# Kernel optimization log

Measured on AMD Instinct MI355X. Metric: run time of the kernel, lower is better.

## Reference

```python
import jax, jax.numpy as jnp
import numpy as np

N = 256          # num agents
HID = 128        # hidden_dim
ACT = 5          # action_dim
NH = 4           # num_heads
D = HID + 16     # concat_hidden_dim = 144
E = D * NH       # mha embed dim = 576
HD = D           # per-head dim = E // NH = 144
OBS_RX, OBS_RY = 4, 2   # obs_r from fov_size=(9,5)
GRID = 40


def setup_inputs() -> dict:
    key = jax.random.key(0)
    ks = jax.random.split(key, 24)
    g = lambda k, shape, s: (jax.random.normal(k, shape, dtype=jnp.float32) * s)
    inp = {
        "hidden_state_n": g(ks[0], (N, HID), 1.0),
        "action_n": g(ks[1], (N, HID), 1.0),
        "state_n": jax.random.randint(ks[2], (N, 2), 0, GRID, dtype=jnp.int32),
        # obs encoder
        "W_enc": g(ks[3], (HID, 16), HID ** -0.5), "b_enc": jnp.zeros((16,), jnp.float32),
        # MHABlock outer projections
        "Wq": g(ks[4], (D, E), D ** -0.5), "bq": jnp.zeros((E,), jnp.float32),
        "Wk": g(ks[5], (D, E), D ** -0.5), "bk": jnp.zeros((E,), jnp.float32),
        "Wv": g(ks[6], (D, E), D ** -0.5), "bv": jnp.zeros((E,), jnp.float32),
        # nn.MultiheadAttention internal in/out projections
        "Wiq": g(ks[7], (E, E), E ** -0.5), "biq": jnp.zeros((E,), jnp.float32),
        "Wik": g(ks[8], (E, E), E ** -0.5), "bik": jnp.zeros((E,), jnp.float32),
        "Wiv": g(ks[9], (E, E), E ** -0.5), "biv": jnp.zeros((E,), jnp.float32),
        "Wo_proj": g(ks[10], (E, E), E ** -0.5), "bo_proj": jnp.zeros((E,), jnp.float32),
        "W_O": g(ks[11], (E, D), E ** -0.5),  # no bias
        # dueling decoders
        "W_val": g(ks[12], (D, 1), D ** -0.5), "b_val": jnp.zeros((1,), jnp.float32),
        "W_adv": g(ks[13], (D, ACT), D ** -0.5), "b_adv": jnp.zeros((ACT,), jnp.float32),
    }
    return inp


def reference(hidden_state_n, action_n, W_enc, b_enc, Wq, bq, Wk, bk, Wv, bv,
              Wiq, biq, Wik, bik, Wiv, biv, Wo_proj, bo_proj, W_O,
              W_val, b_val, W_adv, b_adv, state_n):
    n = hidden_state_n.shape[0]
    # observed_agents[i] = {j > i : |x_i-x_j|<=rx and |y_i-y_j|<=ry}
    pos = state_n.astype(jnp.int32)
    dx = jnp.abs(pos[:, None, 0] - pos[None, :, 0])
    dy = jnp.abs(pos[:, None, 1] - pos[None, :, 1])
    upper = jnp.arange(n)[None, :] > jnp.arange(n)[:, None]
    mask = (dx <= OBS_RX) & (dy <= OBS_RY) & upper            # [N,N], mask[i,j]: j observed by i

    # per-neighbor feature c_j = concat(obs_encoder(h_j), a_j)  -> [N, D]
    obs = hidden_state_n @ W_enc + b_enc                       # [N,16]
    C = jnp.concatenate([obs, action_n], axis=-1)              # [N,D]

    # MHABlock: outer Q/K/V projections then nn.MultiheadAttention
    q = (C @ Wq + bq) @ Wiq + biq                              # [N,E]
    k = (C @ Wk + bk) @ Wik + bik
    v = (C @ Wv + bv) @ Wiv + biv
    q2 = q.reshape(n, NH, HD)
    k2 = k.reshape(n, NH, HD)
    v2 = v.reshape(n, NH, HD)

    scale = 1.0 / np.sqrt(HD).astype(np.float32)
    S = jnp.einsum("jhd,khd->hjk", q2, k2) * scale             # [H,N,N] shared across agents

    pair = (mask[:, None, :, None] & mask[:, None, None, :])   # [N,1,Nq,Nk]
    logits = jnp.where(pair, S[None, :, :, :], -1e9)           # [N,H,N,N]
    m = jnp.max(logits, axis=-1, keepdims=True)
    p = jnp.exp(logits - m) * pair.astype(logits.dtype)
    attn = p / jnp.maximum(p.sum(axis=-1, keepdims=True), 1e-9)

    ctx = jnp.einsum("ihjk,khd->ijhd", attn, v2).reshape(n, n, E)  # [N,Nq,E]
    out = (ctx @ Wo_proj + bo_proj) @ W_O                          # [N,Nq,D]

    # sum over the (masked) neighbor/query axis -> per-agent h_i
    h = jnp.sum(out * mask[:, :, None].astype(out.dtype), axis=1)  # [N,D]

    V = h @ W_val + b_val                                          # [N,1]
    A = h @ W_adv + b_adv                                          # [N,ACT]
    Q = V + A - jnp.mean(A, axis=-1, keepdims=True)                # dueling Q
    return Q
```

## Files before the change

kernel.cpp:

```cpp
#include <hip/hip_runtime.h>
#include <hip/hip_bf16.h>

#define NAG 256
#define HID 128
#define ACT 5
#define NH 4
#define DD 144
#define EE 576
#define HDIM 144
#define CMAX 20

template<int KDIM, int AG, int NX, int GSLOTS>
__global__ __launch_bounds__(256) void k_gemmK(
    const float* __restrict__ A0, const float* __restrict__ A1, const float* __restrict__ A2,
    const float* __restrict__ W0, const float* __restrict__ W1, const float* __restrict__ W2,
    const float* __restrict__ bb0, const float* __restrict__ bb1, const float* __restrict__ bb2,
    const float* __restrict__ bscale,
    float* __restrict__ o0, float* __restrict__ o1, float* __restrict__ o2,
    int N)
{
    constexpr int Kc = KDIM / 4;
    constexpr int G  = 36;
    constexpr int NG = Kc / G;
    constexpr int LDA = KDIM + 4;
    __shared__ union { float As[8 * LDA]; float red[2048]; } sm;

    const int p = blockIdx.x;
    const int xcd = p & 7, qq = p >> 3;
    const int mb = qq & 31, gslot = qq >> 5;
    const int g = xcd + 8 * gslot;
    if (g >= AG) return;
    const int bx = g % NX, z = g / NX;
    const float* A   = (z == 0) ? A0  : (z == 1) ? A1  : A2;
    const float* W   = (z == 0) ? W0  : (z == 1) ? W1  : W2;
    const float* bia = (z == 0) ? bb0 : (z == 1) ? bb1 : bb2;
    float*       out = (z == 0) ? o0  : (z == 1) ? o1  : o2;
    const int tid = threadIdx.x;

    for (int idx = tid; idx < 8 * (KDIM / 4); idx += 256) {
        int r = idx / (KDIM / 4), c = idx % (KDIM / 4);
        *((float4*)&sm.As[r * LDA + c * 4]) =
            *(const float4*)(A + (size_t)(mb * 8 + r) * KDIM + c * 4);
    }
    __syncthreads();

    const int wave = tid >> 6, lane = tid & 63;
    const int colg = bx * 64 + lane;
    const bool cv = colg < N;
    const int colc = cv ? colg : (N - 1);
    const float* Wp = W + (size_t)(wave * Kc) * N + colc;
    float acc[8] = {};
    float wv[G], wn[G];
    #pragma unroll
    for (int j = 0; j < G; ++j) wv[j] = Wp[(size_t)j * N];
    for (int gi = 0; gi < NG; ++gi) {
        if (gi + 1 < NG) {
            const float* Wn = Wp + (size_t)(gi + 1) * G * N;
            #pragma unroll
            for (int j = 0; j < G; ++j) wn[j] = Wn[(size_t)j * N];
        }
        const int kb = wave * Kc + gi * G;
        #pragma unroll
        for (int j4 = 0; j4 < G / 4; ++j4) {
            #pragma unroll
            for (int r = 0; r < 8; ++r) {
                float4 a4 = *(const float4*)&sm.As[r * LDA + kb + j4 * 4];
                acc[r] += a4.x * wv[j4 * 4 + 0] + a4.y * wv[j4 * 4 + 1]
                        + a4.z * wv[j4 * 4 + 2] + a4.w * wv[j4 * 4 + 3];
            }
        }
        #pragma unroll
        for (int j = 0; j < G; ++j) wv[j] = wn[j];
    }
    __syncthreads();
    #pragma unroll
    for (int r = 0; r < 8; ++r) sm.red[wave * 512 + r * 64 + lane] = acc[r];
    __syncthreads();
    #pragma unroll
    for (int q = 0; q < 2; ++q) {
        int idx = tid + q * 256;
        int r = idx >> 6, cl = idx & 63;
        int col = bx * 64 + cl;
        if (col < N) {
            float s = sm.red[idx] + sm.red[512 + idx]
                    + sm.red[1024 + idx] + sm.red[1536 + idx];
            int row = mb * 8 + r;
            float bs = bscale ? bscale[row] : 1.f;
            float bb = bia ? bia[col] : 0.f;
            out[(size_t)row * N + col] = s + bs * bb;
        }
    }
}

__global__ __launch_bounds__(256) void k_gemm1(
    const float* __restrict__ hidden, const float* __restrict__ action,
    const float* __restrict__ W_enc, const float* __restrict__ b_enc,
    const float* __restrict__ Wq, const float* __restrict__ Wk, const float* __restrict__ Wv,
    const float* __restrict__ bq, const float* __restrict__ bk, const float* __restrict__ bv,
    float* __restrict__ tq, float* __restrict__ tk, float* __restrict__ tv)
{
    const int p = blockIdx.x;
    const int xcd = p & 7, qq = p >> 3;
    const int mb = qq & 31, gslot = qq >> 5;
    const int g = xcd + 8 * gslot;
    if (g >= 27) return;
    const int bx = g % 9, z = g / 9;
    const float* W  = (z == 0) ? Wq : (z == 1) ? Wk : Wv;
    const float* bi = (z == 0) ? bq : (z == 1) ? bk : bv;
    float*      out = (z == 0) ? tq : (z == 1) ? tk : tv;
    const int tid = threadIdx.x;

    __shared__ float Ct[8][148];
    __shared__ union { struct { float Hs[8][132]; float We[2048]; } e;
                       float red[2048]; } u;
    {
        int r = tid >> 5, kq = tid & 31;
        *((float4*)&u.e.Hs[r][kq * 4]) =
            *(const float4*)(hidden + (mb * 8 + r) * HID + kq * 4);
        *((float4*)&Ct[r][16 + kq * 4]) =
            *(const float4*)(action + (mb * 8 + r) * HID + kq * 4);
        *((float4*)&u.e.We[tid * 4])        = *(const float4*)(W_enc + tid * 4);
        *((float4*)&u.e.We[1024 + tid * 4]) = *(const float4*)(W_enc + 1024 + tid * 4);
    }
    __syncthreads();
    if (tid < 128) {
        int r = tid >> 4, o = tid & 15;
        float acc = 0.f;
        #pragma unroll 8
        for (int d = 0; d < HID; ++d) acc += u.e.Hs[r][d] * u.e.We[d * 16 + o];
        Ct[r][o] = acc + b_enc[o];
    }
    __syncthreads();

    constexpr int Kc = 36, G = 36;
    const int wave = tid >> 6, lane = tid & 63;
    const int colg = bx * 64 + lane;
    const float* Wp = W + (size_t)(wave * Kc) * EE + colg;
    float acc[8] = {};
    float wv[G];
    #pragma unroll
    for (int j = 0; j < G; ++j) wv[j] = Wp[(size_t)j * EE];
    const int kb = wave * Kc;
    #pragma unroll
    for (int j4 = 0; j4 < G / 4; ++j4) {
        #pragma unroll
        for (int r = 0; r < 8; ++r) {
            float4 a4 = *(const float4*)&Ct[r][kb + j4 * 4];
            acc[r] += a4.x * wv[j4 * 4 + 0] + a4.y * wv[j4 * 4 + 1]
                    + a4.z * wv[j4 * 4 + 2] + a4.w * wv[j4 * 4 + 3];
        }
    }
    __syncthreads();
    #pragma unroll
    for (int r = 0; r < 8; ++r) u.red[wave * 512 + r * 64 + lane] = acc[r];
    __syncthreads();
    #pragma unroll
    for (int q = 0; q < 2; ++q) {
        int idx = tid + q * 256;
        int r = idx >> 6, cl = idx & 63;
        int col = bx * 64 + cl;
        float s = u.red[idx] + u.red[512 + idx]
                + u.red[1024 + idx] + u.red[1536 + idx];
        out[(size_t)(mb * 8 + r) * EE + col] = s + bi[col];
    }
}

__global__ __launch_bounds__(256) void k_attn(
    const int* __restrict__ state, const float* __restrict__ q,
    const float* __restrict__ kmat, const float* __restrict__ v,
    float* __restrict__ ctxsum, float* __restrict__ cnt)
{
    __shared__ int lst[NAG];
    __shared__ int cnt_s;
    __shared__ float w4[NH][NAG];
    __shared__ float qh[CMAX][HDIM + 1];
    __shared__ float kh[CMAX][HDIM + 1];
    __shared__ float Sl[CMAX][CMAX + 1];
    const int i = blockIdx.x, tid = threadIdx.x;
    if (tid == 0) cnt_s = 0;
    __syncthreads();
    {
        int xi = state[2 * i], yi = state[2 * i + 1];
        int xj = state[2 * tid], yj = state[2 * tid + 1];
        int dx = xi - xj; if (dx < 0) dx = -dx;
        int dy = yi - yj; if (dy < 0) dy = -dy;
        if (tid > i && dx <= 4 && dy <= 2) {
            int p = atomicAdd(&cnt_s, 1);
            lst[p] = tid;
        }
    }
    __syncthreads();
    const int c = cnt_s;
    if (tid == 0) cnt[i] = (float)c;
    if (c == 0) {
        for (int e = tid; e < EE; e += 256) ctxsum[i * EE + e] = 0.f;
        return;
    }
    if (c <= CMAX) {
        for (int h = 0; h < NH; ++h) {
            for (int idx = tid; idx < c * HDIM; idx += 256) {
                int jj = idx / HDIM, d = idx % HDIM;
                qh[jj][d] = q[lst[jj] * EE + h * HDIM + d];
                kh[jj][d] = kmat[lst[jj] * EE + h * HDIM + d];
            }
            __syncthreads();
            for (int pp = tid; pp < c * c; pp += 256) {
                int jj = pp / c, kk = pp % c;
                float acc = 0.f;
                for (int d = 0; d < HDIM; ++d) acc += qh[jj][d] * kh[kk][d];
                Sl[jj][kk] = acc * (1.0f / 12.0f);
            }
            __syncthreads();
            if (tid < c) {
                float m = -1e30f;
                for (int kk = 0; kk < c; ++kk) m = fmaxf(m, Sl[tid][kk]);
                float zz = 0.f;
                for (int kk = 0; kk < c; ++kk) zz += __expf(Sl[tid][kk] - m);
                float inv = 1.f / fmaxf(zz, 1e-9f);
                for (int kk = 0; kk < c; ++kk)
                    Sl[tid][kk] = __expf(Sl[tid][kk] - m) * inv;
            }
            __syncthreads();
            if (tid < c) {
                float s = 0.f;
                for (int jj = 0; jj < c; ++jj) s += Sl[jj][tid];
                w4[h][tid] = s;
            }
            __syncthreads();
        }
    } else {
        for (int idx = tid; idx < NH * c; idx += 256) w4[idx / c][idx % c] = 0.f;
        __syncthreads();
        for (int pnh = tid; pnh < NH * c; pnh += 256) {
            int h = pnh / c, jj = pnh % c;
            const float* qrow = q + lst[jj] * EE + h * HDIM;
            float m = -1e30f;
            for (int kk = 0; kk < c; ++kk) {
                const float* krow = kmat + lst[kk] * EE + h * HDIM;
                float a = 0.f;
                for (int d = 0; d < HDIM; ++d) a += qrow[d] * krow[d];
                m = fmaxf(m, a * (1.0f / 12.0f));
            }
            float zz = 0.f;
            for (int kk = 0; kk < c; ++kk) {
                const float* krow = kmat + lst[kk] * EE + h * HDIM;
                float a = 0.f;
                for (int d = 0; d < HDIM; ++d) a += qrow[d] * krow[d];
                zz += __expf(a * (1.0f / 12.0f) - m);
            }
            float inv = 1.f / fmaxf(zz, 1e-9f);
            for (int kk = 0; kk < c; ++kk) {
                const float* krow = kmat + lst[kk] * EE + h * HDIM;
                float a = 0.f;
                for (int d = 0; d < HDIM; ++d) a += qrow[d] * krow[d];
                atomicAdd(&w4[h][kk], __expf(a * (1.0f / 12.0f) - m) * inv);
            }
        }
        __syncthreads();
    }
    for (int e = tid; e < EE; e += 256) {
        int h = e / HDIM;
        float a0 = 0.f, a1 = 0.f;
        int t = 0;
        for (; t + 1 < c; t += 2) {
            a0 += w4[h][t] * v[lst[t] * EE + e];
            a1 += w4[h][t + 1] * v[lst[t + 1] * EE + e];
        }
        if (t < c) a0 += w4[h][t] * v[lst[t] * EE + e];
        ctxsum[i * EE + e] = a0 + a1;
    }
}

__global__ __launch_bounds__(64) void k_head(
    const float* __restrict__ hb,
    const float* __restrict__ W_val, const float* __restrict__ b_val,
    const float* __restrict__ W_adv, const float* __restrict__ b_adv,
    float* __restrict__ out)
{
    const int i = blockIdx.x, t = threadIdx.x;
    const float* hr = hb + i * DD;
    float h0 = hr[t], h1 = hr[t + 64];
    float h2 = (t < 16) ? hr[t + 128] : 0.f;
    float red[6];
    for (int o = 0; o < 6; ++o) {
        float p;
        if (o < 5) {
            p = h0 * W_adv[t * ACT + o] + h1 * W_adv[(t + 64) * ACT + o];
            if (t < 16) p += h2 * W_adv[(t + 128) * ACT + o];
        } else {
            p = h0 * W_val[t] + h1 * W_val[t + 64];
            if (t < 16) p += h2 * W_val[t + 128];
        }
        for (int off = 32; off; off >>= 1) p += __shfl_xor(p, off);
        red[o] = p;
    }
    if (t == 0) {
        float a[ACT], mean = 0.f;
        for (int o = 0; o < ACT; ++o) { a[o] = red[o] + b_adv[o]; mean += a[o]; }
        mean *= (1.0f / ACT);
        float V = red[5] + b_val[0];
        for (int o = 0; o < ACT; ++o) out[i * ACT + o] = V + a[o] - mean;
    }
}

extern "C" void kernel_launch(void* const* d_in, const int* in_sizes, int n_in,
                              void* d_out, int out_size, void* d_ws, size_t ws_size,
                              hipStream_t stream)
{
    const float* hidden = (const float*)d_in[0];
    const float* action = (const float*)d_in[1];
    const int*   state  = (const int*)d_in[2];

    float* ws = (float*)d_ws;
    float* tq   = ws;
    float* tk   = tq   + NAG * EE;
    float* tv   = tk   + NAG * EE;
    float* q    = tv   + NAG * EE;
    float* kb   = q    + NAG * EE;
    float* v    = kb   + NAG * EE;
    float* ctx  = v    + NAG * EE;
    float* cnt  = ctx  + NAG * EE;
    float* hbuf = cnt  + NAG;
    float* tout = tq;

    k_gemm1<<<1024, 256, 0, stream>>>(hidden, action,
        (const float*)d_in[3], (const float*)d_in[4],
        (const float*)d_in[5], (const float*)d_in[7], (const float*)d_in[9],
        (const float*)d_in[6], (const float*)d_in[8], (const float*)d_in[10],
        tq, tk, tv);

    k_gemmK<576, 27, 9, 4><<<1024, 256, 0, stream>>>(tq, tk, tv,
        (const float*)d_in[11], (const float*)d_in[13], (const float*)d_in[15],
        (const float*)d_in[12], (const float*)d_in[14], (const float*)d_in[16],
        nullptr, q, kb, v, EE);

    k_attn<<<NAG, 256, 0, stream>>>(state, q, kb, v, ctx, cnt);

    k_gemmK<576, 9, 9, 2><<<512, 256, 0, stream>>>(ctx, ctx, ctx,
        (const float*)d_in[17], (const float*)d_in[17], (const float*)d_in[17],
        (const float*)d_in[18], (const float*)d_in[18], (const float*)d_in[18],
        cnt, tout, tout, tout, EE);

    k_gemmK<576, 3, 3, 1><<<256, 256, 0, stream>>>(tout, tout, tout,
        (const float*)d_in[19], (const float*)d_in[19], (const float*)d_in[19],
        nullptr, nullptr, nullptr,
        nullptr, hbuf, hbuf, hbuf, DD);

    k_head<<<NAG, 64, 0, stream>>>(hbuf,
        (const float*)d_in[20], (const float*)d_in[21],
        (const float*)d_in[22], (const float*)d_in[23], (float*)d_out);
}
```

Baseline: 194.7 us.

## Convert large weights to bf16 in spare gemm1 blocks and fuse W_O with head

```diff
diff --git a/kernel.cpp b/kernel.cpp
--- a/kernel.cpp
+++ b/kernel.cpp
@@ -1,5 +1,7 @@
 #include <hip/hip_runtime.h>
 #include <hip/hip_bf16.h>
+
+typedef __hip_bfloat16 bf16;
 
 #define NAG 256
 #define HID 128
@@ -13,7 +15,7 @@
 template<int KDIM, int AG, int NX, int GSLOTS>
 __global__ __launch_bounds__(256) void k_gemmK(
     const float* __restrict__ A0, const float* __restrict__ A1, const float* __restrict__ A2,
-    const float* __restrict__ W0, const float* __restrict__ W1, const float* __restrict__ W2,
+    const bf16* __restrict__ W0, const bf16* __restrict__ W1, const bf16* __restrict__ W2,
     const float* __restrict__ bb0, const float* __restrict__ bb1, const float* __restrict__ bb2,
     const float* __restrict__ bscale,
     float* __restrict__ o0, float* __restrict__ o1, float* __restrict__ o2,
@@ -32,7 +34,7 @@
     if (g >= AG) return;
     const int bx = g % NX, z = g / NX;
     const float* A   = (z == 0) ? A0  : (z == 1) ? A1  : A2;
-    const float* W   = (z == 0) ? W0  : (z == 1) ? W1  : W2;
+    const bf16*  W   = (z == 0) ? W0  : (z == 1) ? W1  : W2;
     const float* bia = (z == 0) ? bb0 : (z == 1) ? bb1 : bb2;
     float*       out = (z == 0) ? o0  : (z == 1) ? o1  : o2;
     const int tid = threadIdx.x;
@@ -48,16 +50,16 @@
     const int colg = bx * 64 + lane;
     const bool cv = colg < N;
     const int colc = cv ? colg : (N - 1);
-    const float* Wp = W + (size_t)(wave * Kc) * N + colc;
+    const bf16* Wp = W + (size_t)(wave * Kc) * N + colc;
     float acc[8] = {};
     float wv[G], wn[G];
     #pragma unroll
-    for (int j = 0; j < G; ++j) wv[j] = Wp[(size_t)j * N];
+    for (int j = 0; j < G; ++j) wv[j] = __bfloat162float(Wp[(size_t)j * N]);
     for (int gi = 0; gi < NG; ++gi) {
         if (gi + 1 < NG) {
-            const float* Wn = Wp + (size_t)(gi + 1) * G * N;
+            const bf16* Wn = Wp + (size_t)(gi + 1) * G * N;
             #pragma unroll
-            for (int j = 0; j < G; ++j) wn[j] = Wn[(size_t)j * N];
+            for (int j = 0; j < G; ++j) wn[j] = __bfloat162float(Wn[(size_t)j * N]);
         }
         const int kb = wave * Kc + gi * G;
         #pragma unroll
@@ -97,18 +99,34 @@
     const float* __restrict__ W_enc, const float* __restrict__ b_enc,
     const float* __restrict__ Wq, const float* __restrict__ Wk, const float* __restrict__ Wv,
     const float* __restrict__ bq, const float* __restrict__ bk, const float* __restrict__ bv,
-    float* __restrict__ tq, float* __restrict__ tk, float* __restrict__ tv)
+    const float* __restrict__ Wiq, const float* __restrict__ Wik, const float* __restrict__ Wiv,
+    const float* __restrict__ Wo, const float* __restrict__ W_O,
+    float* __restrict__ tq, float* __restrict__ tk, float* __restrict__ tv,
+    bf16* __restrict__ Wbiq, bf16* __restrict__ Wbik, bf16* __restrict__ Wbiv,
+    bf16* __restrict__ Wbo, bf16* __restrict__ WbO)
 {
     const int p = blockIdx.x;
     const int xcd = p & 7, qq = p >> 3;
     const int mb = qq & 31, gslot = qq >> 5;
     const int g = xcd + 8 * gslot;
-    if (g >= 27) return;
+    const int tid = threadIdx.x;
+    if (g >= 27) {
+        const int wb = (g - 27) * 32 + mb;
+        const int CH = 8832;
+        for (int i = wb * CH + tid; i < (wb + 1) * CH; i += 256) {
+            if (i >= 1410048) break;
+            if (i < 331776)        Wbiq[i]           = __float2bfloat16(Wiq[i]);
+            else if (i < 663552)   Wbik[i - 331776]  = __float2bfloat16(Wik[i - 331776]);
+            else if (i < 995328)   Wbiv[i - 663552]  = __float2bfloat16(Wiv[i - 663552]);
+            else if (i < 1327104)  Wbo[i - 995328]   = __float2bfloat16(Wo[i - 995328]);
+            else                   WbO[i - 1327104]  = __float2bfloat16(W_O[i - 1327104]);
+        }
+        return;
+    }
     const int bx = g % 9, z = g / 9;
     const float* W  = (z == 0) ? Wq : (z == 1) ? Wk : Wv;
     const float* bi = (z == 0) ? bq : (z == 1) ? bk : bv;
     float*      out = (z == 0) ? tq : (z == 1) ? tk : tv;
-    const int tid = threadIdx.x;
 
     __shared__ float Ct[8][148];
     __shared__ union { struct { float Hs[8][132]; float We[2048]; } e;
@@ -271,35 +289,70 @@
     }
 }
 
-__global__ __launch_bounds__(64) void k_head(
-    const float* __restrict__ hb,
+__global__ __launch_bounds__(256) void k_tail(
+    const float* __restrict__ tout, const bf16* __restrict__ WbO,
     const float* __restrict__ W_val, const float* __restrict__ b_val,
     const float* __restrict__ W_adv, const float* __restrict__ b_adv,
     float* __restrict__ out)
 {
-    const int i = blockIdx.x, t = threadIdx.x;
-    const float* hr = hb + i * DD;
-    float h0 = hr[t], h1 = hr[t + 64];
-    float h2 = (t < 16) ? hr[t + 128] : 0.f;
+    __shared__ float As[4][EE];
+    __shared__ float hb[4][DD];
+    const int b = blockIdx.x, tid = threadIdx.x;
+    const int a0 = b * 4;
+    for (int idx = tid; idx < 4 * (EE / 4); idx += 256) {
+        int r = idx / (EE / 4), c4 = idx % (EE / 4);
+        *((float4*)&As[r][c4 * 4]) =
+            *(const float4*)(tout + (size_t)(a0 + r) * EE + c4 * 4);
+    }
+    __syncthreads();
+    if (tid < DD) {
+        const int col = tid;
+        const bf16* Wp = WbO + col;
+        float ac0 = 0.f, ac1 = 0.f, ac2 = 0.f, ac3 = 0.f;
+        float wv[32], wn[32];
+        #pragma unroll
+        for (int j = 0; j < 32; ++j) wv[j] = __bfloat162float(Wp[(size_t)j * DD]);
+        for (int gI = 0; gI < 18; ++gI) {
+            if (gI + 1 < 18) {
+                const bf16* Wn = Wp + (size_t)(gI + 1) * 32 * DD;
+                #pragma unroll
+                for (int j = 0; j < 32; ++j) wn[j] = __bfloat162float(Wn[(size_t)j * DD]);
+            }
+            const int kb = gI * 32;
+            #pragma unroll
+            for (int j = 0; j < 32; ++j) {
+                float w = wv[j];
+                ac0 += As[0][kb + j] * w; ac1 += As[1][kb + j] * w;
+                ac2 += As[2][kb + j] * w; ac3 += As[3][kb + j] * w;
+            }
+            #pragma unroll
+            for (int j = 0; j < 32; ++j) wv[j] = wn[j];
+        }
+        hb[0][col] = ac0; hb[1][col] = ac1; hb[2][col] = ac2; hb[3][col] = ac3;
+    }
+    __syncthreads();
+    const int wave = tid >> 6, lane = tid & 63;
+    float h0 = hb[wave][lane], h1 = hb[wave][lane + 64];
+    float h2 = (lane < 16) ? hb[wave][lane + 128] : 0.f;
     float red[6];
     for (int o = 0; o < 6; ++o) {
         float p;
         if (o < 5) {
-            p = h0 * W_adv[t * ACT + o] + h1 * W_adv[(t + 64) * ACT + o];
-            if (t < 16) p += h2 * W_adv[(t + 128) * ACT + o];
+            p = h0 * W_adv[lane * ACT + o] + h1 * W_adv[(lane + 64) * ACT + o];
+            if (lane < 16) p += h2 * W_adv[(lane + 128) * ACT + o];
         } else {
-            p = h0 * W_val[t] + h1 * W_val[t + 64];
-            if (t < 16) p += h2 * W_val[t + 128];
+            p = h0 * W_val[lane] + h1 * W_val[lane + 64];
+            if (lane < 16) p += h2 * W_val[lane + 128];
         }
         for (int off = 32; off; off >>= 1) p += __shfl_xor(p, off);
         red[o] = p;
     }
-    if (t == 0) {
+    if (lane == 0) {
         float a[ACT], mean = 0.f;
         for (int o = 0; o < ACT; ++o) { a[o] = red[o] + b_adv[o]; mean += a[o]; }
         mean *= (1.0f / ACT);
         float V = red[5] + b_val[0];
-        for (int o = 0; o < ACT; ++o) out[i * ACT + o] = V + a[o] - mean;
+        for (int o = 0; o < ACT; ++o) out[(a0 + wave) * ACT + o] = V + a[o] - mean;
     }
 }
 
@@ -320,33 +373,35 @@
     float* v    = kb   + NAG * EE;
     float* ctx  = v    + NAG * EE;
     float* cnt  = ctx  + NAG * EE;
-    float* hbuf = cnt  + NAG;
+    bf16*  bw   = (bf16*)(cnt + NAG);
+    bf16*  Wbiq = bw;
+    bf16*  Wbik = Wbiq + 331776;
+    bf16*  Wbiv = Wbik + 331776;
+    bf16*  Wbo  = Wbiv + 331776;
+    bf16*  WbO  = Wbo  + 331776;
     float* tout = tq;
 
     k_gemm1<<<1024, 256, 0, stream>>>(hidden, action,
         (const float*)d_in[3], (const float*)d_in[4],
         (const float*)d_in[5], (const float*)d_in[7], (const float*)d_in[9],
         (const float*)d_in[6], (const float*)d_in[8], (const float*)d_in[10],
-        tq, tk, tv);
+        (const float*)d_in[11], (const float*)d_in[13], (const float*)d_in[15],
+        (const float*)d_in[17], (const float*)d_in[19],
+        tq, tk, tv, Wbiq, Wbik, Wbiv, Wbo, WbO);
 
     k_gemmK<576, 27, 9, 4><<<1024, 256, 0, stream>>>(tq, tk, tv,
-        (const float*)d_in[11], (const float*)d_in[13], (const float*)d_in[15],
+        Wbiq, Wbik, Wbiv,
         (const float*)d_in[12], (const float*)d_in[14], (const float*)d_in[16],
         nullptr, q, kb, v, EE);
 
     k_attn<<<NAG, 256, 0, stream>>>(state, q, kb, v, ctx, cnt);
 
     k_gemmK<576, 9, 9, 2><<<512, 256, 0, stream>>>(ctx, ctx, ctx,
-        (const float*)d_in[17], (const float*)d_in[17], (const float*)d_in[17],
+        Wbo, Wbo, Wbo,
         (const float*)d_in[18], (const float*)d_in[18], (const float*)d_in[18],
         cnt, tout, tout, tout, EE);
 
-    k_gemmK<576, 3, 3, 1><<<256, 256, 0, stream>>>(tout, tout, tout,
-        (const float*)d_in[19], (const float*)d_in[19], (const float*)d_in[19],
-        nullptr, nullptr, nullptr,
-        nullptr, hbuf, hbuf, hbuf, DD);
-
-    k_head<<<NAG, 64, 0, stream>>>(hbuf,
+    k_tail<<<64, 256, 0, stream>>>(tout, WbO,
         (const float*)d_in[20], (const float*)d_in[21],
         (const float*)d_in[22], (const float*)d_in[23], (float*)d_out);
 }
```

Measured after the change: 212.6 us. 1.09x slower.
